# Kernel optimization log

Hardware: AMD Instinct MI355X
Metric: run time of the kernel (lower is better)

The kernel has to match this reference:

```python
import jax, jax.numpy as jnp
import numpy as np

B, T, E, U, V = 512, 256, 256, 512, 10000


def _lstm_scan(x_seq, Wx, Wh, b, reverse=False):
    # x_seq: [B, T, E]; returns final (h, c), each [B, U]
    def step(carry, x_t):
        h, c = carry
        gates = x_t @ Wx + h @ Wh + b  # [B, 4U]
        i, f, g, o = jnp.split(gates, 4, axis=-1)
        i = jax.nn.sigmoid(i)
        f = jax.nn.sigmoid(f)
        o = jax.nn.sigmoid(o)
        g = jnp.tanh(g)
        c = f * c + i * g
        h = o * jnp.tanh(c)
        return (h, c), None

    init = (jnp.zeros((x_seq.shape[0], U), x_seq.dtype),
            jnp.zeros((x_seq.shape[0], U), x_seq.dtype))
    xs = jnp.swapaxes(x_seq, 0, 1)  # [T, B, E]
    (h, c), _ = jax.lax.scan(step, init, xs, reverse=reverse)
    return h, c


def setup_inputs() -> dict:
    key = jax.random.key(0)
    ks = jax.random.split(key, 12)
    s = lambda k, shape, scale: jax.random.normal(k, shape, jnp.float32) * scale
    return {
        "sentence": jax.random.randint(ks[0], (B, T), 0, V),
        "emb": s(ks[1], (V, E), 0.05),
        "Wx_fw": s(ks[2], (E, 4 * U), 1.0 / np.sqrt(E)),
        "Wh_fw": s(ks[3], (U, 4 * U), 1.0 / np.sqrt(U)),
        "b_fw": jnp.zeros((4 * U,), jnp.float32),
        "Wx_bw": s(ks[4], (E, 4 * U), 1.0 / np.sqrt(E)),
        "Wh_bw": s(ks[5], (U, 4 * U), 1.0 / np.sqrt(U)),
        "b_bw": jnp.zeros((4 * U,), jnp.float32),
        "W1": s(ks[6], (2 * U, 64), 1.0 / np.sqrt(2 * U)),
        "b1": jnp.zeros((64,), jnp.float32),
        "W2": s(ks[7], (64, V), 1.0 / np.sqrt(64)),
        "b2": jnp.zeros((V,), jnp.float32),
    }


def reference(sentence, emb, Wx_fw, Wh_fw, b_fw, Wx_bw, Wh_bw, b_bw, W1, b1, W2, b2):
    x = emb[sentence]  # [B, T, E]
    h_fw, _ = _lstm_scan(x, Wx_fw, Wh_fw, b_fw, reverse=False)
    # backward loop iterates t = T-1 .. 0, i.e. consumes the sequence reversed
    h_bw, _ = _lstm_scan(x, Wx_bw, Wh_bw, b_bw, reverse=True)
    h = jnp.concatenate([h_fw, h_bw], axis=-1)  # [B, 2U]
    hidden = jax.nn.relu(h @ W1 + b1)
    return jax.nn.softmax(hidden @ W2 + b2, axis=-1)
```

## Files before the change

### kernel.cpp

```cpp
#include <hip/hip_runtime.h>

#define Bb 512
#define Tt 256
#define Ee 256
#define Uu 512
#define Vv 10000

#define PACKB_OFF 0
#define HBUF_OFF  6291456
#define CBUF_OFF  8388608
#define HID_OFF   10485760

typedef __attribute__((ext_vector_type(8))) short short8;
typedef __attribute__((ext_vector_type(4))) float f32x4;

__device__ __forceinline__ float bf2f(ushort u) {
  union { unsigned int i; float f; } v; v.i = ((unsigned int)u) << 16; return v.f;
}
__device__ __forceinline__ ushort f2bf(float f) {
  union { float f; unsigned int i; } v; v.f = f;
  unsigned int x = v.i;
  return (ushort)((x + 0x7fffu + ((x >> 16) & 1u)) >> 16);
}
__device__ __forceinline__ float fast_sigmoid(float x) {
  return 1.f / (1.f + __expf(-x));
}
__device__ __forceinline__ float fast_tanh(float x) {
  float t = __expf(-2.f * fabsf(x));
  float r = (1.f - t) / (1.f + t);
  return x >= 0.f ? r : -r;
}

__global__ __launch_bounds__(256) void init_zero(char* ob)
{
  uint4 z; z.x = 0; z.y = 0; z.z = 0; z.w = 0;
  ((uint4*)(ob + HBUF_OFF))[(size_t)blockIdx.x * 256 + threadIdx.x] = z;
}

__global__ __launch_bounds__(256) void pack_weights(
    const float* __restrict__ Wx_fw, const float* __restrict__ Wh_fw,
    const float* __restrict__ Wx_bw, const float* __restrict__ Wh_bw,
    char* ob)
{
  __shared__ ushort tile[32][520];
  ushort* packB = (ushort*)(ob + PACKB_OFF);
  const int cq = blockIdx.x;
  const int ks = blockIdx.y;
  const int d  = blockIdx.z;
  const int tid = threadIdx.x;
  const float* Wx = d ? Wx_bw : Wx_fw;
  const float* Wh = d ? Wh_bw : Wh_fw;
  const int colbase = cq * 512;

  #pragma unroll
  for (int i = 0; i < 8; i++) {
    int chunk = tid + i * 256;
    int row = chunk >> 6;
    int cc = (chunk & 63) * 8;
    int k = ks * 32 + row;
    const float* src = (k < Ee) ? (Wx + (size_t)k * 2048 + colbase + cc)
                                : (Wh + (size_t)(k - Ee) * 2048 + colbase + cc);
    f32x4 f0 = *(const f32x4*)src;
    f32x4 f1 = *(const f32x4*)(src + 4);
    #pragma unroll
    for (int j = 0; j < 4; j++) {
      tile[row][cc + j]     = f2bf(f0[j]);
      tile[row][cc + 4 + j] = f2bf(f1[j]);
    }
  }
  __syncthreads();
  #pragma unroll
  for (int i = 0; i < 8; i++) {
    int chunk = tid + i * 256;
    int ctl = chunk >> 6;
    int lane = chunk & 63;
    int quad = lane >> 4, l15 = lane & 15;
    short8 v;
    #pragma unroll
    for (int jj = 0; jj < 8; jj++)
      v[jj] = (short)tile[quad * 8 + jj][ctl * 16 + l15];
    int ct = (colbase >> 4) + ctl;
    *(short8*)(packB + (((size_t)(d * 128 + ct) * 24 + ks) * 512) + lane * 8) = v;
  }
}

__global__ __launch_bounds__(256) void lstm_step(
    char* ob,
    const int*   __restrict__ sent,
    const float* __restrict__ emb,
    const float* __restrict__ b_fw,
    const float* __restrict__ b_bw,
    int s)
{
  const ushort* packB = (const ushort*)(ob + PACKB_OFF);
  ushort* hbuf = (ushort*)(ob + HBUF_OFF);
  float*  cbuf = (float*)(ob + CBUF_OFF);

  const int ut = blockIdx.x;
  const int bt = blockIdx.y;
  const int d  = blockIdx.z;
  const int tid = threadIdx.x;
  const int w = tid >> 6;
  const int lane = tid & 63;
  const int l15 = lane & 15, quad = lane >> 4;
  const int b0 = bt * 64;
  const int t = d ? (Tt - 1 - s) : s;

  const int mrow = b0 + w * 16 + l15;
  const int tok = sent[mrow * Tt + t];

  const ushort* hread  = hbuf + (size_t)((s & 1) * 2 + d) * Bb * Uu;
  ushort*       hwrite = hbuf + (size_t)((((s & 1) ^ 1) * 2) + d) * Bb * Uu;

  const float*  aemb = emb + (size_t)tok * Ee + quad * 8;
  const ushort* ah   = hread + (size_t)mrow * Uu + quad * 8;

  const ushort* bbase[2][4];
  #pragma unroll
  for (int j = 0; j < 2; j++)
    #pragma unroll
    for (int q = 0; q < 4; q++)
      bbase[j][q] = packB + ((size_t)(d * 128 + q * 32 + ut * 2 + j) * 24) * 512 + lane * 8;

  f32x4 acc[2][4];
  #pragma unroll
  for (int j = 0; j < 2; j++)
    #pragma unroll
    for (int q = 0; q < 4; q++)
      acc[j][q] = (f32x4){0.f, 0.f, 0.f, 0.f};

  #pragma unroll
  for (int ks = 0; ks < 8; ks++) {
    f32x4 f0 = *(const f32x4*)(aemb + ks * 32);
    f32x4 f1 = *(const f32x4*)(aemb + ks * 32 + 4);
    short8 a;
    #pragma unroll
    for (int j = 0; j < 4; j++) {
      a[j]     = (short)f2bf(f0[j]);
      a[4 + j] = (short)f2bf(f1[j]);
    }
    #pragma unroll
    for (int j = 0; j < 2; j++)
      #pragma unroll
      for (int q = 0; q < 4; q++) {
        short8 bv = *(const short8*)(bbase[j][q] + ks * 512);
        acc[j][q] = __builtin_amdgcn_mfma_f32_16x16x32_bf16(a, bv, acc[j][q], 0, 0, 0);
      }
  }
  #pragma unroll
  for (int ks = 8; ks < 24; ks++) {
    short8 a = *(const short8*)(ah + (ks - 8) * 32);
    #pragma unroll
    for (int j = 0; j < 2; j++)
      #pragma unroll
      for (int q = 0; q < 4; q++) {
        short8 bv = *(const short8*)(bbase[j][q] + ks * 512);
        acc[j][q] = __builtin_amdgcn_mfma_f32_16x16x32_bf16(a, bv, acc[j][q], 0, 0, 0);
      }
  }

  const float* bias = d ? b_bw : b_fw;
  #pragma unroll
  for (int j = 0; j < 2; j++) {
    int u = ut * 32 + j * 16 + l15;
    float bi  = bias[u];
    float bff = bias[512 + u];
    float bg  = bias[1024 + u];
    float bo  = bias[1536 + u];
    #pragma unroll
    for (int r = 0; r < 4; r++) {
      int m = b0 + w * 16 + quad * 4 + r;
      float iv = fast_sigmoid(acc[j][0][r] + bi);
      float fv = fast_sigmoid(acc[j][1][r] + bff);
      float gv = fast_tanh(acc[j][2][r] + bg);
      float ov = fast_sigmoid(acc[j][3][r] + bo);
      size_t cidx = ((size_t)d * Bb + m) * Uu + u;
      float cn = fv * cbuf[cidx] + iv * gv;
      cbuf[cidx] = cn;
      hwrite[(size_t)m * Uu + u] = f2bf(ov * fast_tanh(cn));
    }
  }
}

__global__ __launch_bounds__(256) void hidden_kernel(
    char* ob, const float* __restrict__ W1, const float* __restrict__ b1)
{
  const ushort* hbuf = (const ushort*)(ob + HBUF_OFF);
  float* hidden = (float*)(ob + HID_OFF);
  int m = blockIdx.x * 4 + (threadIdx.x >> 6);
  int col = threadIdx.x & 63;
  const ushort* hf = hbuf + (size_t)m * Uu;
  const ushort* hb = hbuf + (size_t)(Bb + m) * Uu;
  float acc = b1[col];
  for (int k = 0; k < 512; k++) acc += bf2f(hf[k]) * W1[k * 64 + col];
  for (int k = 0; k < 512; k++) acc += bf2f(hb[k]) * W1[(512 + k) * 64 + col];
  hidden[(size_t)m * 64 + col] = fmaxf(acc, 0.f);
}

__device__ __forceinline__ void softmax_row(
    const float* hs, const float* __restrict__ W2, const float* __restrict__ b2,
    float* out, int m, float* red)
{
  const int tid = threadIdx.x;
  float lg[40];
  float mx = -1e30f;
  #pragma unroll 4
  for (int i = 0; i < 40; i++) {
    int c = tid + i * 256;
    float a = -1e30f;
    if (c < Vv) {
      a = b2[c];
      for (int k = 0; k < 64; k++) a += hs[k] * W2[(size_t)k * Vv + c];
    }
    lg[i] = a;
    mx = fmaxf(mx, a);
  }
  red[tid] = mx; __syncthreads();
  for (int off = 128; off > 0; off >>= 1) {
    if (tid < off) red[tid] = fmaxf(red[tid], red[tid + off]);
    __syncthreads();
  }
  mx = red[0];
  __syncthreads();

  float sum = 0.f;
  #pragma unroll 4
  for (int i = 0; i < 40; i++) {
    int c = tid + i * 256;
    if (c < Vv) { lg[i] = __expf(lg[i] - mx); sum += lg[i]; }
  }
  red[tid] = sum; __syncthreads();
  for (int off = 128; off > 0; off >>= 1) {
    if (tid < off) red[tid] += red[tid + off];
    __syncthreads();
  }
  float inv = 1.f / red[0];
  __syncthreads();
  #pragma unroll 4
  for (int i = 0; i < 40; i++) {
    int c = tid + i * 256;
    if (c < Vv) out[(size_t)m * Vv + c] = lg[i] * inv;
  }
}

__global__ __launch_bounds__(256) void logits_main(
    char* ob, const float* __restrict__ W2, const float* __restrict__ b2)
{
  __shared__ float hs[64];
  __shared__ float red[256];
  const float* hidden = (const float*)(ob + HID_OFF);
  float* out = (float*)ob;
  int bx = blockIdx.x;
  int m = (bx < 262) ? bx : (bx + 4);
  if (threadIdx.x < 64) hs[threadIdx.x] = hidden[(size_t)m * 64 + threadIdx.x];
  __syncthreads();
  softmax_row(hs, W2, b2, out, m, red);
}

__global__ __launch_bounds__(256) void logits_tail(
    char* ob, const float* __restrict__ W2, const float* __restrict__ b2)
{
  __shared__ float hs4[4][64];
  __shared__ float red[256];
  const float* hidden = (const float*)(ob + HID_OFF);
  float* out = (float*)ob;
  if (threadIdx.x < 256) {
    int r = threadIdx.x >> 6, col = threadIdx.x & 63;
    hs4[r][col] = hidden[(size_t)(262 + r) * 64 + col];
  }
  __syncthreads();
  for (int r = 0; r < 4; r++) {
    softmax_row(hs4[r], W2, b2, out, 262 + r, red);
    __syncthreads();
  }
}

extern "C" void kernel_launch(void* const* d_in, const int* in_sizes, int n_in,
                              void* d_out, int out_size, void* d_ws, size_t ws_size,
                              hipStream_t stream)
{
  const int*   sent  = (const int*)d_in[0];
  const float* emb   = (const float*)d_in[1];
  const float* Wx_fw = (const float*)d_in[2];
  const float* Wh_fw = (const float*)d_in[3];
  const float* b_fw  = (const float*)d_in[4];
  const float* Wx_bw = (const float*)d_in[5];
  const float* Wh_bw = (const float*)d_in[6];
  const float* b_bw  = (const float*)d_in[7];
  const float* W1    = (const float*)d_in[8];
  const float* b1    = (const float*)d_in[9];
  const float* W2    = (const float*)d_in[10];
  const float* b2    = (const float*)d_in[11];
  char* ob = (char*)d_out;
  (void)d_ws; (void)ws_size; (void)in_sizes; (void)n_in; (void)out_size;

  init_zero<<<1024, 256, 0, stream>>>(ob);
  pack_weights<<<dim3(4, 24, 2), 256, 0, stream>>>(Wx_fw, Wh_fw, Wx_bw, Wh_bw, ob);

  for (int s = 0; s < Tt; s++)
    lstm_step<<<dim3(16, 8, 2), 256, 0, stream>>>(ob, sent, emb, b_fw, b_bw, s);

  hidden_kernel<<<128, 256, 0, stream>>>(ob, W1, b1);

  logits_main<<<508, 256, 0, stream>>>(ob, W2, b2);
  logits_tail<<<1,   256, 0, stream>>>(ob, W2, b2);
}
```

Before: 5.119 ms.

## Replace per-step LSTM launches with persistent kernel using atomic counter barriers

Result: faster. 4.251 ms (-17.0%).

```diff
diff --git a/kernel.cpp b/kernel.cpp
--- a/kernel.cpp
+++ b/kernel.cpp
@@ -8,8 +8,9 @@
 
 #define PACKB_OFF 0
 #define HBUF_OFF  6291456
-#define CBUF_OFF  8388608
-#define HID_OFF   10485760
+#define HID_OFF   8388608
+#define CNT_OFF   8519680
+#define EMB_OFF   12582912
 
 typedef __attribute__((ext_vector_type(8))) short short8;
 typedef __attribute__((ext_vector_type(4))) float f32x4;
@@ -31,10 +32,39 @@
   return x >= 0.f ? r : -r;
 }
 
+__device__ __forceinline__ short8 load_h16(const ushort* p) {
+  union { unsigned long long u[2]; short8 s; } v;
+  v.u[0] = __hip_atomic_load((const unsigned long long*)p,     __ATOMIC_RELAXED, __HIP_MEMORY_SCOPE_AGENT);
+  v.u[1] = __hip_atomic_load((const unsigned long long*)p + 1, __ATOMIC_RELAXED, __HIP_MEMORY_SCOPE_AGENT);
+  return v.s;
+}
+__device__ __forceinline__ void store_h(ushort* p, ushort v) {
+  __hip_atomic_store(p, v, __ATOMIC_RELAXED, __HIP_MEMORY_SCOPE_AGENT);
+}
+
 __global__ __launch_bounds__(256) void init_zero(char* ob)
 {
-  uint4 z; z.x = 0; z.y = 0; z.z = 0; z.w = 0;
-  ((uint4*)(ob + HBUF_OFF))[(size_t)blockIdx.x * 256 + threadIdx.x] = z;
+  if (blockIdx.x < 512) {
+    uint4 z; z.x = 0; z.y = 0; z.z = 0; z.w = 0;
+    ((uint4*)(ob + HBUF_OFF))[(size_t)blockIdx.x * 256 + threadIdx.x] = z;
+  } else {
+    ((unsigned int*)(ob + CNT_OFF))[threadIdx.x] = 0u;
+  }
+}
+
+__global__ __launch_bounds__(256) void conv_emb(const float* __restrict__ emb, char* ob)
+{
+  ushort* embB = (ushort*)(ob + EMB_OFF);
+  size_t i = ((size_t)blockIdx.x * 256 + threadIdx.x) * 8;
+  f32x4 f0 = *(const f32x4*)(emb + i);
+  f32x4 f1 = *(const f32x4*)(emb + i + 4);
+  short8 v;
+  #pragma unroll
+  for (int j = 0; j < 4; j++) {
+    v[j]     = (short)f2bf(f0[j]);
+    v[4 + j] = (short)f2bf(f1[j]);
+  }
+  *(short8*)(embB + i) = v;
 }
 
 __global__ __launch_bounds__(256) void pack_weights(
@@ -84,101 +114,134 @@
   }
 }
 
-__global__ __launch_bounds__(256) void lstm_step(
-    char* ob,
-    const int*   __restrict__ sent,
-    const float* __restrict__ emb,
-    const float* __restrict__ b_fw,
-    const float* __restrict__ b_bw,
-    int s)
-{
+__global__ __launch_bounds__(256) void lstm_persistent(
+    char* ob, const int* __restrict__ sent,
+    const float* __restrict__ b_fw, const float* __restrict__ b_bw)
+{
+  __shared__ ushort ldsB[32768];
   const ushort* packB = (const ushort*)(ob + PACKB_OFF);
+  const ushort* embB  = (const ushort*)(ob + EMB_OFF);
   ushort* hbuf = (ushort*)(ob + HBUF_OFF);
-  float*  cbuf = (float*)(ob + CBUF_OFF);
-
-  const int ut = blockIdx.x;
-  const int bt = blockIdx.y;
-  const int d  = blockIdx.z;
+
+  const int utp = blockIdx.x;
+  const int bt  = blockIdx.y;
+  const int d   = blockIdx.z;
+  unsigned int* cnt = (unsigned int*)(ob + CNT_OFF) + (d * 4 + bt) * 32;
+
   const int tid = threadIdx.x;
-  const int w = tid >> 6;
-  const int lane = tid & 63;
+  const int w = tid >> 6, lane = tid & 63;
   const int l15 = lane & 15, quad = lane >> 4;
-  const int b0 = bt * 64;
-  const int t = d ? (Tt - 1 - s) : s;
-
-  const int mrow = b0 + w * 16 + l15;
-  const int tok = sent[mrow * Tt + t];
-
-  const ushort* hread  = hbuf + (size_t)((s & 1) * 2 + d) * Bb * Uu;
-  ushort*       hwrite = hbuf + (size_t)((((s & 1) ^ 1) * 2) + d) * Bb * Uu;
-
-  const float*  aemb = emb + (size_t)tok * Ee + quad * 8;
-  const ushort* ah   = hread + (size_t)mrow * Uu + quad * 8;
-
-  const ushort* bbase[2][4];
-  #pragma unroll
-  for (int j = 0; j < 2; j++)
-    #pragma unroll
-    for (int q = 0; q < 4; q++)
-      bbase[j][q] = packB + ((size_t)(d * 128 + q * 32 + ut * 2 + j) * 24) * 512 + lane * 8;
-
-  f32x4 acc[2][4];
-  #pragma unroll
-  for (int j = 0; j < 2; j++)
-    #pragma unroll
-    for (int q = 0; q < 4; q++)
-      acc[j][q] = (f32x4){0.f, 0.f, 0.f, 0.f};
-
-  #pragma unroll
-  for (int ks = 0; ks < 8; ks++) {
-    f32x4 f0 = *(const f32x4*)(aemb + ks * 32);
-    f32x4 f1 = *(const f32x4*)(aemb + ks * 32 + 4);
-    short8 a;
-    #pragma unroll
-    for (int j = 0; j < 4; j++) {
-      a[j]     = (short)f2bf(f0[j]);
-      a[4 + j] = (short)f2bf(f1[j]);
-    }
-    #pragma unroll
-    for (int j = 0; j < 2; j++)
+  const int mbase = bt * 128 + w * 32;
+  const int u = utp * 16 + l15;
+
+  for (int i = 0; i < 16; i++) {
+    int c = tid + i * 256;
+    int lc = c & 63, qc = (c >> 6) & 3, k8 = c >> 8;
+    const ushort* src = packB +
+        ((size_t)(d * 128 + qc * 32 + utp) * 24 + 8 + k8) * 512 + lc * 8;
+    *(short8*)&ldsB[(k8 * 4 + qc) * 512 + lc * 8] = *(const short8*)src;
+  }
+
+  const float* bias = d ? b_bw : b_fw;
+  const float bi  = bias[u];
+  const float bfv = bias[512 + u];
+  const float bg  = bias[1024 + u];
+  const float bo  = bias[1536 + u];
+
+  const ushort* bembP[4];
+  #pragma unroll
+  for (int q = 0; q < 4; q++)
+    bembP[q] = packB + ((size_t)(d * 128 + q * 32 + utp) * 24) * 512 + lane * 8;
+
+  float creg[2][4];
+  #pragma unroll
+  for (int a = 0; a < 2; a++)
+    #pragma unroll
+    for (int r = 0; r < 4; r++) creg[a][r] = 0.f;
+
+  __syncthreads();
+
+  for (int s = 0; s < Tt; s++) {
+    const int t = d ? (Tt - 1 - s) : s;
+    const ushort* hread  = hbuf + (size_t)((s & 1) * 2 + d) * Bb * Uu;
+    ushort*       hwrite = hbuf + (size_t)((((s & 1) ^ 1) * 2) + d) * Bb * Uu;
+
+    f32x4 acc[2][4];
+    #pragma unroll
+    for (int a = 0; a < 2; a++)
       #pragma unroll
-      for (int q = 0; q < 4; q++) {
-        short8 bv = *(const short8*)(bbase[j][q] + ks * 512);
-        acc[j][q] = __builtin_amdgcn_mfma_f32_16x16x32_bf16(a, bv, acc[j][q], 0, 0, 0);
+      for (int q = 0; q < 4; q++)
+        acc[a][q] = (f32x4){0.f, 0.f, 0.f, 0.f};
+
+    const int tok0 = sent[(mbase + l15) * Tt + t];
+    const int tok1 = sent[(mbase + 16 + l15) * Tt + t];
+    const ushort* e0 = embB + (size_t)tok0 * Ee + quad * 8;
+    const ushort* e1 = embB + (size_t)tok1 * Ee + quad * 8;
+
+    #pragma unroll
+    for (int ks = 0; ks < 8; ks++) {
+      short8 bq0 = *(const short8*)(bembP[0] + ks * 512);
+      short8 bq1 = *(const short8*)(bembP[1] + ks * 512);
+      short8 bq2 = *(const short8*)(bembP[2] + ks * 512);
+      short8 bq3 = *(const short8*)(bembP[3] + ks * 512);
+      short8 a0 = *(const short8*)(e0 + ks * 32);
+      short8 a1 = *(const short8*)(e1 + ks * 32);
+      acc[0][0] = __builtin_amdgcn_mfma_f32_16x16x32_bf16(a0, bq0, acc[0][0], 0, 0, 0);
+      acc[0][1] = __builtin_amdgcn_mfma_f32_16x16x32_bf16(a0, bq1, acc[0][1], 0, 0, 0);
+      acc[0][2] = __builtin_amdgcn_mfma_f32_16x16x32_bf16(a0, bq2, acc[0][2], 0, 0, 0);
+      acc[0][3] = __builtin_amdgcn_mfma_f32_16x16x32_bf16(a0, bq3, acc[0][3], 0, 0, 0);
+      acc[1][0] = __builtin_amdgcn_mfma_f32_16x16x32_bf16(a1, bq0, acc[1][0], 0, 0, 0);
+      acc[1][1] = __builtin_amdgcn_mfma_f32_16x16x32_bf16(a1, bq1, acc[1][1], 0, 0, 0);
+      acc[1][2] = __builtin_amdgcn_mfma_f32_16x16x32_bf16(a1, bq2, acc[1][2], 0, 0, 0);
+      acc[1][3] = __builtin_amdgcn_mfma_f32_16x16x32_bf16(a1, bq3, acc[1][3], 0, 0, 0);
+    }
+
+    if (tid == 0) {
+      const unsigned int target = 32u * (unsigned int)s;
+      while (__hip_atomic_fetch_add(cnt, 0u, __ATOMIC_RELAXED,
+                                    __HIP_MEMORY_SCOPE_AGENT) < target)
+        __builtin_amdgcn_s_sleep(2);
+    }
+    __syncthreads();
+
+    const ushort* h0 = hread + (size_t)(mbase + l15) * Uu + quad * 8;
+    const ushort* h1 = hread + (size_t)(mbase + 16 + l15) * Uu + quad * 8;
+    #pragma unroll
+    for (int k8 = 0; k8 < 16; k8++) {
+      short8 bq0 = *(const short8*)&ldsB[(k8 * 4 + 0) * 512 + lane * 8];
+      short8 bq1 = *(const short8*)&ldsB[(k8 * 4 + 1) * 512 + lane * 8];
+      short8 bq2 = *(const short8*)&ldsB[(k8 * 4 + 2) * 512 + lane * 8];
+      short8 bq3 = *(const short8*)&ldsB[(k8 * 4 + 3) * 512 + lane * 8];
+      short8 a0 = load_h16(h0 + k8 * 32);
+      short8 a1 = load_h16(h1 + k8 * 32);
+      acc[0][0] = __builtin_amdgcn_mfma_f32_16x16x32_bf16(a0, bq0, acc[0][0], 0, 0, 0);
+      acc[0][1] = __builtin_amdgcn_mfma_f32_16x16x32_bf16(a0, bq1, acc[0][1], 0, 0, 0);
+      acc[0][2] = __builtin_amdgcn_mfma_f32_16x16x32_bf16(a0, bq2, acc[0][2], 0, 0, 0);
+      acc[0][3] = __builtin_amdgcn_mfma_f32_16x16x32_bf16(a0, bq3, acc[0][3], 0, 0, 0);
+      acc[1][0] = __builtin_amdgcn_mfma_f32_16x16x32_bf16(a1, bq0, acc[1][0], 0, 0, 0);
+      acc[1][1] = __builtin_amdgcn_mfma_f32_16x16x32_bf16(a1, bq1, acc[1][1], 0, 0, 0);
+      acc[1][2] = __builtin_amdgcn_mfma_f32_16x16x32_bf16(a1, bq2, acc[1][2], 0, 0, 0);
+      acc[1][3] = __builtin_amdgcn_mfma_f32_16x16x32_bf16(a1, bq3, acc[1][3], 0, 0, 0);
+    }
+
+    #pragma unroll
+    for (int a = 0; a < 2; a++) {
+      #pragma unroll
+      for (int r = 0; r < 4; r++) {
+        float iv = fast_sigmoid(acc[a][0][r] + bi);
+        float fv = fast_sigmoid(acc[a][1][r] + bfv);
+        float gv = fast_tanh(acc[a][2][r] + bg);
+        float ov = fast_sigmoid(acc[a][3][r] + bo);
+        float cn = fv * creg[a][r] + iv * gv;
+        creg[a][r] = cn;
+        int m = mbase + a * 16 + quad * 4 + r;
+        store_h(hwrite + (size_t)m * Uu + u, f2bf(ov * fast_tanh(cn)));
       }
-  }
-  #pragma unroll
-  for (int ks = 8; ks < 24; ks++) {
-    short8 a = *(const short8*)(ah + (ks - 8) * 32);
-    #pragma unroll
-    for (int j = 0; j < 2; j++)
-      #pragma unroll
-      for (int q = 0; q < 4; q++) {
-        short8 bv = *(const short8*)(bbase[j][q] + ks * 512);
-        acc[j][q] = __builtin_amdgcn_mfma_f32_16x16x32_bf16(a, bv, acc[j][q], 0, 0, 0);
-      }
-  }
-
-  const float* bias = d ? b_bw : b_fw;
-  #pragma unroll
-  for (int j = 0; j < 2; j++) {
-    int u = ut * 32 + j * 16 + l15;
-    float bi  = bias[u];
-    float bff = bias[512 + u];
-    float bg  = bias[1024 + u];
-    float bo  = bias[1536 + u];
-    #pragma unroll
-    for (int r = 0; r < 4; r++) {
-      int m = b0 + w * 16 + quad * 4 + r;
-      float iv = fast_sigmoid(acc[j][0][r] + bi);
-      float fv = fast_sigmoid(acc[j][1][r] + bff);
-      float gv = fast_tanh(acc[j][2][r] + bg);
-      float ov = fast_sigmoid(acc[j][3][r] + bo);
-      size_t cidx = ((size_t)d * Bb + m) * Uu + u;
-      float cn = fv * cbuf[cidx] + iv * gv;
-      cbuf[cidx] = cn;
-      hwrite[(size_t)m * Uu + u] = f2bf(ov * fast_tanh(cn));
-    }
+    }
+
+    __syncthreads();
+    if (tid == 0)
+      __hip_atomic_fetch_add(cnt, 1u, __ATOMIC_RELAXED, __HIP_MEMORY_SCOPE_AGENT);
   }
 }
 
@@ -251,7 +314,7 @@
   const float* hidden = (const float*)(ob + HID_OFF);
   float* out = (float*)ob;
   int bx = blockIdx.x;
-  int m = (bx < 262) ? bx : (bx + 4);
+  int m = (bx < 209) ? bx : (bx + 4);
   if (threadIdx.x < 64) hs[threadIdx.x] = hidden[(size_t)m * 64 + threadIdx.x];
   __syncthreads();
   softmax_row(hs, W2, b2, out, m, red);
@@ -264,13 +327,13 @@
   __shared__ float red[256];
   const float* hidden = (const float*)(ob + HID_OFF);
   float* out = (float*)ob;
-  if (threadIdx.x < 256) {
+  {
     int r = threadIdx.x >> 6, col = threadIdx.x & 63;
-    hs4[r][col] = hidden[(size_t)(262 + r) * 64 + col];
+    hs4[r][col] = hidden[(size_t)(209 + r) * 64 + col];
   }
   __syncthreads();
   for (int r = 0; r < 4; r++) {
-    softmax_row(hs4[r], W2, b2, out, 262 + r, red);
+    softmax_row(hs4[r], W2, b2, out, 209 + r, red);
     __syncthreads();
   }
 }
@@ -294,14 +357,13 @@
   char* ob = (char*)d_out;
   (void)d_ws; (void)ws_size; (void)in_sizes; (void)n_in; (void)out_size;
 
-  init_zero<<<1024, 256, 0, stream>>>(ob);
+  init_zero<<<513, 256, 0, stream>>>(ob);
   pack_weights<<<dim3(4, 24, 2), 256, 0, stream>>>(Wx_fw, Wh_fw, Wx_bw, Wh_bw, ob);
-
-  for (int s = 0; s < Tt; s++)
-    lstm_step<<<dim3(16, 8, 2), 256, 0, stream>>>(ob, sent, emb, b_fw, b_bw, s);
+  conv_emb<<<1250, 256, 0, stream>>>(emb, ob);
+
+  lstm_persistent<<<dim3(32, 4, 2), 256, 0, stream>>>(ob, sent, b_fw, b_bw);
 
   hidden_kernel<<<128, 256, 0, stream>>>(ob, W1, b1);
-
   logits_main<<<508, 256, 0, stream>>>(ob, W2, b2);
   logits_tail<<<1,   256, 0, stream>>>(ob, W2, b2);
 }
```
